# Optimization experiments

Measured on AMD Instinct MI355X. Metric: run time of the kernel, lower is better.

## Reference

```python
import jax, jax.numpy as jnp
import numpy as np

B, T, A, H = 2048, 512, 32, 16


def setup_inputs() -> dict:
    key = jax.random.key(0)
    ks = jax.random.split(key, 10)
    s = 1.0 / np.sqrt(H)
    inputs = jax.random.normal(ks[0], (B, T, A), dtype=jnp.float32)
    masks = (jax.random.uniform(ks[1], (B, T)) > 0.05).astype(jnp.float32)
    h0 = jnp.zeros((1, B, H), dtype=jnp.float32)
    c0 = jnp.zeros((1, B, H), dtype=jnp.float32)
    # torch nn.LSTM params (gate order i,f,g,o) and linear heads
    w_ih = jax.random.uniform(ks[2], (4 * H, A), minval=-s, maxval=s)
    w_hh = jax.random.uniform(ks[3], (4 * H, H), minval=-s, maxval=s)
    b_ih = jax.random.uniform(ks[4], (4 * H,), minval=-s, maxval=s)
    b_hh = jax.random.uniform(ks[5], (4 * H,), minval=-s, maxval=s)
    w_actor = jax.random.uniform(ks[6], (A, H), minval=-s, maxval=s)
    b_actor = jax.random.uniform(ks[7], (A,), minval=-s, maxval=s)
    w_critic = jax.random.uniform(ks[8], (1, H), minval=-s, maxval=s)
    b_critic = jax.random.uniform(ks[9], (1,), minval=-s, maxval=s)
    return {"inputs": inputs, "masks": masks, "h0": h0, "c0": c0,
            "w_ih": w_ih, "w_hh": w_hh, "b_ih": b_ih, "b_hh": b_hh,
            "w_actor": w_actor, "b_actor": b_actor,
            "w_critic": w_critic, "b_critic": b_critic}


def reference(inputs, masks, h0, c0, w_ih, w_hh, b_ih, b_hh,
              w_actor, b_actor, w_critic, b_critic):
    # masked LSTM scan: state is zeroed where mask==0 before each step
    def step(carry, xm):
        h, c = carry                      # [B,H]
        x, m = xm                         # x:[B,A], m:[B]
        h = h * m[:, None]
        c = c * m[:, None]
        gates = x @ w_ih.T + b_ih + h @ w_hh.T + b_hh   # [B,4H]
        i, f, g, o = jnp.split(gates, 4, axis=-1)
        i = jax.nn.sigmoid(i)
        f = jax.nn.sigmoid(f)
        g = jnp.tanh(g)
        o = jax.nn.sigmoid(o)
        c2 = f * c + i * g
        h2 = o * jnp.tanh(c2)
        return (h2, c2), h2

    xs = (jnp.swapaxes(inputs, 0, 1), masks.T)          # time-major
    (hT, cT), feats = jax.lax.scan(step, (h0[0], c0[0]), xs)
    feats = jnp.swapaxes(feats, 0, 1)                   # [B,T,H]
    actor = feats @ w_actor.T + b_actor                 # [B,T,A]
    critic = feats @ w_critic.T + b_critic              # [B,T,1]
    return actor, critic, hT[None], cT[None]
```

## Files before the change

kernel.cpp:

```cpp
#include <hip/hip_runtime.h>
#include <stdint.h>

#define Bn 2048
#define Tn 512
#define An 32
#define Hn 16

typedef __attribute__((ext_vector_type(8))) short bf16x8;
typedef __attribute__((ext_vector_type(4))) float f32x4;

union FragU { bf16x8 v; uint32_t u[4]; };

#define BAR() __asm__ volatile("s_waitcnt lgkmcnt(0)\n\ts_barrier" ::: "memory")

static __device__ __forceinline__ float sigm(float x){
  return __builtin_amdgcn_rcpf(1.0f + __builtin_amdgcn_exp2f(x * -1.44269504088896f));
}
static __device__ __forceinline__ float tanhx(float x){
  return 1.0f - 2.0f * __builtin_amdgcn_rcpf(1.0f + __builtin_amdgcn_exp2f(x * 2.88539008177793f));
}
static __device__ __forceinline__ uint32_t pack_hi16(float a, float b){
  return (__float_as_uint(b) & 0xFFFF0000u) | (__float_as_uint(a) >> 16);
}
static __device__ __forceinline__ void split8(const float* s, FragU& hi, FragU& lo){
#pragma unroll
  for (int d = 0; d < 4; ++d){
    float a = s[2*d], b = s[2*d+1];
    float ah = __uint_as_float(__float_as_uint(a) & 0xFFFF0000u);
    float bh = __uint_as_float(__float_as_uint(b) & 0xFFFF0000u);
    hi.u[d] = pack_hi16(a, b);
    lo.u[d] = pack_hi16(a - ah, b - bh);
  }
}
static __device__ __forceinline__ uint32_t plo(uint32_t e, uint32_t o){
  return __builtin_amdgcn_perm(o, e, 0x05040100u);
}
static __device__ __forceinline__ uint32_t phi(uint32_t e, uint32_t o){
  return __builtin_amdgcn_perm(o, e, 0x07060302u);
}
static __device__ __forceinline__ f32x4 MF(const FragU& a, const FragU& b, f32x4 c){
  return __builtin_amdgcn_mfma_f32_16x16x32_bf16(a.v, b.v, c, 0, 0, 0);
}
static __device__ __forceinline__ void packH(const float* hs, uint32_t* pk){
#pragma unroll
  for (int r = 0; r < 4; ++r){
    float hh_ = __uint_as_float(__float_as_uint(hs[r]) & 0xFFFF0000u);
    pk[r] = (__float_as_uint(hs[r] - hh_) & 0xFFFF0000u) | (__float_as_uint(hs[r]) >> 16);
  }
}
static __device__ __forceinline__ void buildBH(const uint32_t* pk, int srcA, int srcB,
                                               FragU& BHh, FragU& BHl){
  uint32_t d0 = (uint32_t)__builtin_amdgcn_ds_bpermute(srcA, (int)pk[0]);
  uint32_t d1 = (uint32_t)__builtin_amdgcn_ds_bpermute(srcA, (int)pk[1]);
  uint32_t d2 = (uint32_t)__builtin_amdgcn_ds_bpermute(srcA, (int)pk[2]);
  uint32_t d3 = (uint32_t)__builtin_amdgcn_ds_bpermute(srcA, (int)pk[3]);
  uint32_t d4 = (uint32_t)__builtin_amdgcn_ds_bpermute(srcB, (int)pk[0]);
  uint32_t d5 = (uint32_t)__builtin_amdgcn_ds_bpermute(srcB, (int)pk[1]);
  uint32_t d6 = (uint32_t)__builtin_amdgcn_ds_bpermute(srcB, (int)pk[2]);
  uint32_t d7 = (uint32_t)__builtin_amdgcn_ds_bpermute(srcB, (int)pk[3]);
  BHh.u[0] = plo(d0, d1); BHh.u[1] = plo(d2, d3);
  BHh.u[2] = plo(d4, d5); BHh.u[3] = plo(d6, d7);
  BHl.u[0] = phi(d0, d1); BHl.u[1] = phi(d2, d3);
  BHl.u[2] = phi(d4, d5); BHl.u[3] = phi(d6, d7);
}

__global__ __launch_bounds__(256, 1)
void lstm_fused(const float* __restrict__ xin,
                const float* __restrict__ masks,
                const float* __restrict__ h0,
                const float* __restrict__ c0,
                const float* __restrict__ w_ih,
                const float* __restrict__ w_hh,
                const float* __restrict__ b_ih,
                const float* __restrict__ b_hh,
                const float* __restrict__ w_act,
                const float* __restrict__ b_act,
                const float* __restrict__ w_cr,
                const float* __restrict__ b_cr,
                float* __restrict__ actor,
                float* __restrict__ critic,
                float* __restrict__ hT,
                float* __restrict__ cT)
{
  __shared__ float gex[2][4][256];
  __shared__ float mlds[Tn * 16];

  const int tid = threadIdx.x;
  const int w = tid >> 6;
  const int l = tid & 63;
  const int q = l >> 4;
  const int n = l & 15;
  const int b0 = blockIdx.x * 16;
  const int colbase = (q & 1) * 8;
  const bool hiQuad = (q < 2);

  {
    const int rown = (tid >> 4) & 15;
    const int c = tid & 15;
    if (w < 1 || true) {
#pragma unroll
      for (int j = 0; j < 2; ++j){
        int t = c * 32 + j * 16 + ((tid >> 8) & 0);
        (void)t;
      }
    }
    const int row = tid >> 4;
#pragma unroll
    for (int j = 0; j < 8; ++j){
      int t = c * 32 + j * 4;
      float4 v = *(const float4*)&masks[(size_t)(b0 + row) * Tn + t];
      mlds[(t + 0) * 16 + row] = v.x;
      mlds[(t + 1) * 16 + row] = v.y;
      mlds[(t + 2) * 16 + row] = v.z;
      mlds[(t + 3) * 16 + row] = v.w;
    }
  }
  __syncthreads();

  FragU wihH, wihL, whhA1, whhA2;
  f32x4 bias;
  {
    const int g = w;
    float tmp[8];
#pragma unroll
    for (int j = 0; j < 8; ++j) tmp[j] = w_ih[(g*16 + n)*32 + q*8 + j];
    split8(tmp, wihH, wihL);
#pragma unroll
    for (int j = 0; j < 8; ++j) tmp[j] = w_hh[(g*16 + n)*16 + colbase + j];
    FragU hh, hl; split8(tmp, hh, hl);
#pragma unroll
    for (int d = 0; d < 4; ++d){
      whhA1.u[d] = hiQuad ? hh.u[d] : hl.u[d];
      whhA2.u[d] = hiQuad ? hh.u[d] : 0u;
    }
#pragma unroll
    for (int r = 0; r < 4; ++r)
      bias[r] = b_ih[g*16 + q*4 + r] + b_hh[g*16 + q*4 + r];
  }
  FragU whA1, whA2;
  f32x4 biasA;
  float bcr = 0.0f;
  if (w < 2){
    float tmp[8];
#pragma unroll
    for (int j = 0; j < 8; ++j) tmp[j] = w_act[(w*16 + n)*16 + colbase + j];
    FragU hh, hl; split8(tmp, hh, hl);
#pragma unroll
    for (int d = 0; d < 4; ++d){
      whA1.u[d] = hiQuad ? hh.u[d] : hl.u[d];
      whA2.u[d] = hiQuad ? hh.u[d] : 0u;
    }
#pragma unroll
    for (int r = 0; r < 4; ++r) biasA[r] = b_act[w*16 + q*4 + r];
  } else if (w == 2){
    float tmp[8];
#pragma unroll
    for (int j = 0; j < 8; ++j) tmp[j] = (n == 0) ? w_cr[colbase + j] : 0.0f;
    FragU hh, hl; split8(tmp, hh, hl);
#pragma unroll
    for (int d = 0; d < 4; ++d){
      whA1.u[d] = hiQuad ? hh.u[d] : hl.u[d];
      whA2.u[d] = hiQuad ? hh.u[d] : 0u;
    }
    bcr = b_cr[0];
#pragma unroll
    for (int r = 0; r < 4; ++r) biasA[r] = 0.0f;
  }

  const int srcA = (((q & 1) * 2) * 16 + n) * 4;
  const int srcB = srcA + 64;

  float cs[4], hs[4];
#pragma unroll
  for (int r = 0; r < 4; ++r){
    hs[r] = h0[(b0 + n)*16 + q*4 + r];
    cs[r] = c0[(b0 + n)*16 + q*4 + r];
  }
  uint32_t pk[4];
  packH(hs, pk);
  FragU BHh, BHl;
  buildBH(pk, srcA, srcB, BHh, BHl);

  const f32x4 zero4 = {0.f, 0.f, 0.f, 0.f};

  const size_t xrow = (size_t)(b0 + n) * Tn * 32 + q * 8;
  float4 xA[4], xB[4];
#pragma unroll
  for (int u = 0; u < 4; ++u){
    xA[u] = *(const float4*)&xin[xrow + (size_t)u * 32];
    xB[u] = *(const float4*)&xin[xrow + (size_t)u * 32 + 4];
  }
  float mCur = mlds[0 * 16 + n];

  for (int t0 = 0; t0 < Tn; t0 += 4){
#pragma unroll
    for (int u = 0; u < 4; ++u){
      const int t = t0 + u;
      const float m = mCur;
      {
        const int tm = (t + 1 < Tn) ? (t + 1) : t;
        mCur = mlds[tm * 16 + n];
      }

      FragU Xh, Xl;
      {
        float s[8] = {xA[u].x, xA[u].y, xA[u].z, xA[u].w,
                      xB[u].x, xB[u].y, xB[u].z, xB[u].w};
        split8(s, Xh, Xl);
      }
      {
        const int tn = (t + 4 < Tn) ? (t + 4) : t;
        xA[u] = *(const float4*)&xin[xrow + (size_t)tn * 32];
        xB[u] = *(const float4*)&xin[xrow + (size_t)tn * 32 + 4];
      }

      f32x4 ax = MF(wihH, Xh, bias);
      ax = MF(wihH, Xl, ax);
      ax = MF(wihL, Xh, ax);
      f32x4 ah = MF(whhA1, BHh, zero4);
      ah = MF(whhA2, BHl, ah);

      if (t){
        const int th = t - 1;
        if (w < 2){
          f32x4 a = MF(whA1, BHh, biasA);
          a = MF(whA2, BHl, a);
          *(f32x4*)&actor[((size_t)(b0 + n) * Tn + th) * 32 + w*16 + q*4] = a;
        } else if (w == 2){
          f32x4 cc = MF(whA1, BHh, zero4);
          cc = MF(whA2, BHl, cc);
          if (q == 0) critic[(size_t)(b0 + n) * Tn + th] = cc[0] + bcr;
        }
      }

      float own[4];
#pragma unroll
      for (int r = 0; r < 4; ++r){
        float gv = ax[r] + m * ah[r];
        own[r] = (w == 2) ? tanhx(gv) : sigm(gv);
      }

      const int par = t & 1;
      *(float4*)&gex[par][w][l*4] = make_float4(own[0], own[1], own[2], own[3]);
      BAR();
      float4 g0 = *(float4*)&gex[par][0][l*4];
      float4 g1 = *(float4*)&gex[par][1][l*4];
      float4 g2 = *(float4*)&gex[par][2][l*4];
      float4 g3 = *(float4*)&gex[par][3][l*4];
      const float iv[4] = {g0.x, g0.y, g0.z, g0.w};
      const float fv[4] = {g1.x, g1.y, g1.z, g1.w};
      const float gv[4] = {g2.x, g2.y, g2.z, g2.w};
      const float ov[4] = {g3.x, g3.y, g3.z, g3.w};

#pragma unroll
      for (int r = 0; r < 4; ++r){
        float c2 = fv[r] * (cs[r] * m) + iv[r] * gv[r];
        float h2 = ov[r] * tanhx(c2);
        cs[r] = c2;
        hs[r] = h2;
      }
      packH(hs, pk);
      buildBH(pk, srcA, srcB, BHh, BHl);
    }
  }

  {
    const int th = Tn - 1;
    if (w < 2){
      f32x4 a = MF(whA1, BHh, biasA);
      a = MF(whA2, BHl, a);
      *(f32x4*)&actor[((size_t)(b0 + n) * Tn + th) * 32 + w*16 + q*4] = a;
    } else if (w == 2){
      f32x4 cc = MF(whA1, BHh, zero4);
      cc = MF(whA2, BHl, cc);
      if (q == 0) critic[(size_t)(b0 + n) * Tn + th] = cc[0] + bcr;
    }
  }
  if (w == 3){
    *(float4*)&hT[(b0 + n)*16 + q*4] = make_float4(hs[0], hs[1], hs[2], hs[3]);
    *(float4*)&cT[(b0 + n)*16 + q*4] = make_float4(cs[0], cs[1], cs[2], cs[3]);
  }
}

extern "C" void kernel_launch(void* const* d_in, const int* in_sizes, int n_in,
                              void* d_out, int out_size, void* d_ws, size_t ws_size,
                              hipStream_t stream) {
  (void)in_sizes; (void)n_in; (void)out_size; (void)d_ws; (void)ws_size;
  const float* xin   = (const float*)d_in[0];
  const float* masks = (const float*)d_in[1];
  const float* h0    = (const float*)d_in[2];
  const float* c0    = (const float*)d_in[3];
  const float* w_ih  = (const float*)d_in[4];
  const float* w_hh  = (const float*)d_in[5];
  const float* b_ih  = (const float*)d_in[6];
  const float* b_hh  = (const float*)d_in[7];
  const float* w_act = (const float*)d_in[8];
  const float* b_act = (const float*)d_in[9];
  const float* w_cr  = (const float*)d_in[10];
  const float* b_cr  = (const float*)d_in[11];

  float* out    = (float*)d_out;
  float* actor  = out;
  float* critic = out + (size_t)Bn * Tn * An;
  float* hT     = critic + (size_t)Bn * Tn;
  float* cT     = hT + (size_t)Bn * Hn;

  lstm_fused<<<Bn/16, 256, 0, stream>>>(xin, masks, h0, c0, w_ih, w_hh, b_ih, b_hh,
                                        w_act, b_act, w_cr, b_cr,
                                        actor, critic, hT, cT);
}
```

Before: 538.1 us.

## Collapse four gate waves into one wave per block, removing LDS exchange and barriers

Each block now runs a single 64-lane wave that computes all four LSTM gates, the actor heads and the critic head itself. This removes the per-timestep LDS gate exchange and the s_barrier that the four-wave version needed on every recurrent step. The activation scale constants are folded into the weights and biases so sigmoid and tanh reduce to exp2 plus rcp. Masks are read straight from global memory instead of being staged in LDS. In exchange each wave issues four times the MFMA and transcendental work serially, and only 128 waves run across the whole GPU, so latency hiding is weaker.

```diff
diff --git a/kernel.cpp b/kernel.cpp
--- a/kernel.cpp
+++ b/kernel.cpp
@@ -11,14 +11,6 @@
 
 union FragU { bf16x8 v; uint32_t u[4]; };
 
-#define BAR() __asm__ volatile("s_waitcnt lgkmcnt(0)\n\ts_barrier" ::: "memory")
-
-static __device__ __forceinline__ float sigm(float x){
-  return __builtin_amdgcn_rcpf(1.0f + __builtin_amdgcn_exp2f(x * -1.44269504088896f));
-}
-static __device__ __forceinline__ float tanhx(float x){
-  return 1.0f - 2.0f * __builtin_amdgcn_rcpf(1.0f + __builtin_amdgcn_exp2f(x * 2.88539008177793f));
-}
 static __device__ __forceinline__ uint32_t pack_hi16(float a, float b){
   return (__float_as_uint(b) & 0xFFFF0000u) | (__float_as_uint(a) >> 16);
 }
@@ -64,7 +56,7 @@
   BHl.u[2] = phi(d4, d5); BHl.u[3] = phi(d6, d7);
 }
 
-__global__ __launch_bounds__(256, 1)
+__global__ __launch_bounds__(64, 1)
 void lstm_fused(const float* __restrict__ xin,
                 const float* __restrict__ masks,
                 const float* __restrict__ h0,
@@ -82,89 +74,68 @@
                 float* __restrict__ hT,
                 float* __restrict__ cT)
 {
-  __shared__ float gex[2][4][256];
-  __shared__ float mlds[Tn * 16];
-
-  const int tid = threadIdx.x;
-  const int w = tid >> 6;
-  const int l = tid & 63;
+  const int l = threadIdx.x;
   const int q = l >> 4;
   const int n = l & 15;
   const int b0 = blockIdx.x * 16;
   const int colbase = (q & 1) * 8;
   const bool hiQuad = (q < 2);
 
+  const float KS = -1.44269504088896f;
+  const float KG =  2.88539008177793f;
+
+  FragU wihH0, wihL0, whh10, whh20; f32x4 bias0;
+  FragU wihH1, wihL1, whh11, whh21; f32x4 bias1;
+  FragU wihH2, wihL2, whh12, whh22; f32x4 bias2;
+  FragU wihH3, wihL3, whh13, whh23; f32x4 bias3;
   {
-    const int rown = (tid >> 4) & 15;
-    const int c = tid & 15;
-    if (w < 1 || true) {
-#pragma unroll
-      for (int j = 0; j < 2; ++j){
-        int t = c * 32 + j * 16 + ((tid >> 8) & 0);
-        (void)t;
-      }
-    }
-    const int row = tid >> 4;
-#pragma unroll
-    for (int j = 0; j < 8; ++j){
-      int t = c * 32 + j * 4;
-      float4 v = *(const float4*)&masks[(size_t)(b0 + row) * Tn + t];
-      mlds[(t + 0) * 16 + row] = v.x;
-      mlds[(t + 1) * 16 + row] = v.y;
-      mlds[(t + 2) * 16 + row] = v.z;
-      mlds[(t + 3) * 16 + row] = v.w;
-    }
-  }
-  __syncthreads();
-
-  FragU wihH, wihL, whhA1, whhA2;
-  f32x4 bias;
+    auto loadGate = [&](int g, float sc, FragU& wh, FragU& wl, FragU& a1, FragU& a2, f32x4& bg){
+      float tmp[8];
+#pragma unroll
+      for (int j = 0; j < 8; ++j) tmp[j] = w_ih[(g*16 + n)*32 + q*8 + j] * sc;
+      split8(tmp, wh, wl);
+#pragma unroll
+      for (int j = 0; j < 8; ++j) tmp[j] = w_hh[(g*16 + n)*16 + colbase + j] * sc;
+      FragU hh, hl; split8(tmp, hh, hl);
+#pragma unroll
+      for (int d = 0; d < 4; ++d){
+        a1.u[d] = hiQuad ? hh.u[d] : hl.u[d];
+        a2.u[d] = hiQuad ? hh.u[d] : 0u;
+      }
+#pragma unroll
+      for (int r = 0; r < 4; ++r)
+        bg[r] = (b_ih[g*16 + q*4 + r] + b_hh[g*16 + q*4 + r]) * sc;
+    };
+    loadGate(0, KS, wihH0, wihL0, whh10, whh20, bias0);
+    loadGate(1, KS, wihH1, wihL1, whh11, whh21, bias1);
+    loadGate(2, KG, wihH2, wihL2, whh12, whh22, bias2);
+    loadGate(3, KS, wihH3, wihL3, whh13, whh23, bias3);
+  }
+
+  FragU whA10, whA20, whA11, whA21, wcA1, wcA2;
+  f32x4 biasA0, biasA1;
+  const float bcr = b_cr[0];
   {
-    const int g = w;
     float tmp[8];
 #pragma unroll
-    for (int j = 0; j < 8; ++j) tmp[j] = w_ih[(g*16 + n)*32 + q*8 + j];
-    split8(tmp, wihH, wihL);
-#pragma unroll
-    for (int j = 0; j < 8; ++j) tmp[j] = w_hh[(g*16 + n)*16 + colbase + j];
-    FragU hh, hl; split8(tmp, hh, hl);
-#pragma unroll
-    for (int d = 0; d < 4; ++d){
-      whhA1.u[d] = hiQuad ? hh.u[d] : hl.u[d];
-      whhA2.u[d] = hiQuad ? hh.u[d] : 0u;
-    }
-#pragma unroll
-    for (int r = 0; r < 4; ++r)
-      bias[r] = b_ih[g*16 + q*4 + r] + b_hh[g*16 + q*4 + r];
-  }
-  FragU whA1, whA2;
-  f32x4 biasA;
-  float bcr = 0.0f;
-  if (w < 2){
-    float tmp[8];
-#pragma unroll
-    for (int j = 0; j < 8; ++j) tmp[j] = w_act[(w*16 + n)*16 + colbase + j];
-    FragU hh, hl; split8(tmp, hh, hl);
-#pragma unroll
-    for (int d = 0; d < 4; ++d){
-      whA1.u[d] = hiQuad ? hh.u[d] : hl.u[d];
-      whA2.u[d] = hiQuad ? hh.u[d] : 0u;
-    }
-#pragma unroll
-    for (int r = 0; r < 4; ++r) biasA[r] = b_act[w*16 + q*4 + r];
-  } else if (w == 2){
-    float tmp[8];
+    for (int j = 0; j < 8; ++j) tmp[j] = w_act[(0*16 + n)*16 + colbase + j];
+    { FragU hh, hl; split8(tmp, hh, hl);
+#pragma unroll
+      for (int d = 0; d < 4; ++d){ whA10.u[d] = hiQuad ? hh.u[d] : hl.u[d]; whA20.u[d] = hiQuad ? hh.u[d] : 0u; } }
+#pragma unroll
+    for (int r = 0; r < 4; ++r) biasA0[r] = b_act[0*16 + q*4 + r];
+#pragma unroll
+    for (int j = 0; j < 8; ++j) tmp[j] = w_act[(1*16 + n)*16 + colbase + j];
+    { FragU hh, hl; split8(tmp, hh, hl);
+#pragma unroll
+      for (int d = 0; d < 4; ++d){ whA11.u[d] = hiQuad ? hh.u[d] : hl.u[d]; whA21.u[d] = hiQuad ? hh.u[d] : 0u; } }
+#pragma unroll
+    for (int r = 0; r < 4; ++r) biasA1[r] = b_act[1*16 + q*4 + r];
 #pragma unroll
     for (int j = 0; j < 8; ++j) tmp[j] = (n == 0) ? w_cr[colbase + j] : 0.0f;
-    FragU hh, hl; split8(tmp, hh, hl);
-#pragma unroll
-    for (int d = 0; d < 4; ++d){
-      whA1.u[d] = hiQuad ? hh.u[d] : hl.u[d];
-      whA2.u[d] = hiQuad ? hh.u[d] : 0u;
-    }
-    bcr = b_cr[0];
-#pragma unroll
-    for (int r = 0; r < 4; ++r) biasA[r] = 0.0f;
+    { FragU hh, hl; split8(tmp, hh, hl);
+#pragma unroll
+      for (int d = 0; d < 4; ++d){ wcA1.u[d] = hiQuad ? hh.u[d] : hl.u[d]; wcA2.u[d] = hiQuad ? hh.u[d] : 0u; } }
   }
 
   const int srcA = (((q & 1) * 2) * 16 + n) * 4;
@@ -190,7 +161,8 @@
     xA[u] = *(const float4*)&xin[xrow + (size_t)u * 32];
     xB[u] = *(const float4*)&xin[xrow + (size_t)u * 32 + 4];
   }
-  float mCur = mlds[0 * 16 + n];
+  const size_t mrow = (size_t)(b0 + n) * Tn;
+  float mCur = masks[mrow];
 
   for (int t0 = 0; t0 < Tn; t0 += 4){
 #pragma unroll
@@ -199,8 +171,11 @@
       const float m = mCur;
       {
         const int tm = (t + 1 < Tn) ? (t + 1) : t;
-        mCur = mlds[tm * 16 + n];
-      }
+        mCur = masks[mrow + tm];
+      }
+      float cm[4];
+#pragma unroll
+      for (int r = 0; r < 4; ++r) cm[r] = cs[r] * m;
 
       FragU Xh, Xl;
       {
@@ -214,48 +189,41 @@
         xB[u] = *(const float4*)&xin[xrow + (size_t)tn * 32 + 4];
       }
 
-      f32x4 ax = MF(wihH, Xh, bias);
-      ax = MF(wihH, Xl, ax);
-      ax = MF(wihL, Xh, ax);
-      f32x4 ah = MF(whhA1, BHh, zero4);
-      ah = MF(whhA2, BHl, ah);
+      f32x4 ax0 = MF(wihH0, Xh, bias0); ax0 = MF(wihH0, Xl, ax0); ax0 = MF(wihL0, Xh, ax0);
+      f32x4 ax1 = MF(wihH1, Xh, bias1); ax1 = MF(wihH1, Xl, ax1); ax1 = MF(wihL1, Xh, ax1);
+      f32x4 ax2 = MF(wihH2, Xh, bias2); ax2 = MF(wihH2, Xl, ax2); ax2 = MF(wihL2, Xh, ax2);
+      f32x4 ax3 = MF(wihH3, Xh, bias3); ax3 = MF(wihH3, Xl, ax3); ax3 = MF(wihL3, Xh, ax3);
+
+      f32x4 ah0 = MF(whh10, BHh, zero4); ah0 = MF(whh20, BHl, ah0);
+      f32x4 ah1 = MF(whh11, BHh, zero4); ah1 = MF(whh21, BHl, ah1);
+      f32x4 ah2 = MF(whh12, BHh, zero4); ah2 = MF(whh22, BHl, ah2);
+      f32x4 ah3 = MF(whh13, BHh, zero4); ah3 = MF(whh23, BHl, ah3);
 
       if (t){
         const int th = t - 1;
-        if (w < 2){
-          f32x4 a = MF(whA1, BHh, biasA);
-          a = MF(whA2, BHl, a);
-          *(f32x4*)&actor[((size_t)(b0 + n) * Tn + th) * 32 + w*16 + q*4] = a;
-        } else if (w == 2){
-          f32x4 cc = MF(whA1, BHh, zero4);
-          cc = MF(whA2, BHl, cc);
-          if (q == 0) critic[(size_t)(b0 + n) * Tn + th] = cc[0] + bcr;
-        }
-      }
-
-      float own[4];
+        f32x4 a0 = MF(whA10, BHh, biasA0); a0 = MF(whA20, BHl, a0);
+        *(f32x4*)&actor[((size_t)(b0 + n) * Tn + th) * 32 + 0*16 + q*4] = a0;
+        f32x4 a1 = MF(whA11, BHh, biasA1); a1 = MF(whA21, BHl, a1);
+        *(f32x4*)&actor[((size_t)(b0 + n) * Tn + th) * 32 + 1*16 + q*4] = a1;
+        f32x4 cc = MF(wcA1, BHh, zero4); cc = MF(wcA2, BHl, cc);
+        if (q == 0) critic[(size_t)(b0 + n) * Tn + th] = cc[0] + bcr;
+      }
+
 #pragma unroll
       for (int r = 0; r < 4; ++r){
-        float gv = ax[r] + m * ah[r];
-        own[r] = (w == 2) ? tanhx(gv) : sigm(gv);
-      }
-
-      const int par = t & 1;
-      *(float4*)&gex[par][w][l*4] = make_float4(own[0], own[1], own[2], own[3]);
-      BAR();
-      float4 g0 = *(float4*)&gex[par][0][l*4];
-      float4 g1 = *(float4*)&gex[par][1][l*4];
-      float4 g2 = *(float4*)&gex[par][2][l*4];
-      float4 g3 = *(float4*)&gex[par][3][l*4];
-      const float iv[4] = {g0.x, g0.y, g0.z, g0.w};
-      const float fv[4] = {g1.x, g1.y, g1.z, g1.w};
-      const float gv[4] = {g2.x, g2.y, g2.z, g2.w};
-      const float ov[4] = {g3.x, g3.y, g3.z, g3.w};
-
-#pragma unroll
-      for (int r = 0; r < 4; ++r){
-        float c2 = fv[r] * (cs[r] * m) + iv[r] * gv[r];
-        float h2 = ov[r] * tanhx(c2);
+        float gi = ax0[r] + m * ah0[r];
+        float gf = ax1[r] + m * ah1[r];
+        float gg = ax2[r] + m * ah2[r];
+        float go = ax3[r] + m * ah3[r];
+        float iv = __builtin_amdgcn_rcpf(1.0f + __builtin_amdgcn_exp2f(gi));
+        float fv = __builtin_amdgcn_rcpf(1.0f + __builtin_amdgcn_exp2f(gf));
+        float gr = __builtin_amdgcn_rcpf(1.0f + __builtin_amdgcn_exp2f(gg));
+        float ov = __builtin_amdgcn_rcpf(1.0f + __builtin_amdgcn_exp2f(go));
+        float gv = 1.0f - 2.0f * gr;
+        float c2 = fv * cm[r] + iv * gv;
+        float r2 = __builtin_amdgcn_rcpf(1.0f + __builtin_amdgcn_exp2f(c2 * KG));
+        float orr = ov * r2;
+        float h2 = ov - 2.0f * orr;
         cs[r] = c2;
         hs[r] = h2;
       }
@@ -266,20 +234,15 @@
 
   {
     const int th = Tn - 1;
-    if (w < 2){
-      f32x4 a = MF(whA1, BHh, biasA);
-      a = MF(whA2, BHl, a);
-      *(f32x4*)&actor[((size_t)(b0 + n) * Tn + th) * 32 + w*16 + q*4] = a;
-    } else if (w == 2){
-      f32x4 cc = MF(whA1, BHh, zero4);
-      cc = MF(whA2, BHl, cc);
-      if (q == 0) critic[(size_t)(b0 + n) * Tn + th] = cc[0] + bcr;
-    }
-  }
-  if (w == 3){
-    *(float4*)&hT[(b0 + n)*16 + q*4] = make_float4(hs[0], hs[1], hs[2], hs[3]);
-    *(float4*)&cT[(b0 + n)*16 + q*4] = make_float4(cs[0], cs[1], cs[2], cs[3]);
-  }
+    f32x4 a0 = MF(whA10, BHh, biasA0); a0 = MF(whA20, BHl, a0);
+    *(f32x4*)&actor[((size_t)(b0 + n) * Tn + th) * 32 + 0*16 + q*4] = a0;
+    f32x4 a1 = MF(whA11, BHh, biasA1); a1 = MF(whA21, BHl, a1);
+    *(f32x4*)&actor[((size_t)(b0 + n) * Tn + th) * 32 + 1*16 + q*4] = a1;
+    f32x4 cc = MF(wcA1, BHh, zero4); cc = MF(wcA2, BHl, cc);
+    if (q == 0) critic[(size_t)(b0 + n) * Tn + th] = cc[0] + bcr;
+  }
+  *(float4*)&hT[(b0 + n)*16 + q*4] = make_float4(hs[0], hs[1], hs[2], hs[3]);
+  *(float4*)&cT[(b0 + n)*16 + q*4] = make_float4(cs[0], cs[1], cs[2], cs[3]);
 }
 
 extern "C" void kernel_launch(void* const* d_in, const int* in_sizes, int n_in,
@@ -305,7 +268,7 @@
   float* hT     = critic + (size_t)Bn * Tn;
   float* cT     = hT + (size_t)Bn * Hn;
 
-  lstm_fused<<<Bn/16, 256, 0, stream>>>(xin, masks, h0, c0, w_ih, w_hh, b_ih, b_hh,
-                                        w_act, b_act, w_cr, b_cr,
-                                        actor, critic, hT, cT);
-}
+  lstm_fused<<<Bn/16, 64, 0, stream>>>(xin, masks, h0, c0, w_ih, w_hh, b_ih, b_hh,
+                                       w_act, b_act, w_cr, b_cr,
+                                       actor, critic, hT, cT);
+}
```

New measurement: 520.9 us. 3.2% less time.
